# Performance work log

Measured on AMD Instinct MI355X. Metric: run time of the kernel, lower is better.

The kernel has to match this reference:

```python
import jax, jax.numpy as jnp
import numpy as np

B, S, D_IN, D_OUT, K = 4, 4096, 512, 512, 8


def setup_inputs() -> dict:
    key = jax.random.key(0)
    k1, k2, k3, k4 = jax.random.split(key, 4)
    scale_w = 1.0 / np.sqrt(D_IN)
    return {
        "x": jax.random.normal(k1, (B, S, D_IN), dtype=jnp.float32),
        "expert_weights": jax.random.normal(k2, (K, D_OUT, D_IN), dtype=jnp.float32) * scale_w,
        "expert_biases": jax.random.normal(k3, (K, D_OUT), dtype=jnp.float32) * 0.02,
        "mixer_w": jax.random.normal(k4, (K, D_IN), dtype=jnp.float32) * scale_w,
        "mixer_b": jnp.zeros((K,), dtype=jnp.float32),
    }


def reference(x, expert_weights, expert_biases, mixer_w, mixer_b):
    # Gating: coeffs = softmax(mixer(x)) over experts  -> [b, s, k]
    logits = jnp.einsum("bsi,ki->bsk", x, mixer_w) + mixer_b
    coeffs = jax.nn.softmax(logits, axis=-1)
    # Mathematically identical to fusing weights then applying them:
    #   y = einsum('bsi, bsoi -> bso', x, einsum('bsk, koi -> bsoi', coeffs, W))
    # but computed as per-expert GEMM outputs combined by coeffs, avoiding the
    # enormous [b, s, out, in] fused-weight intermediate.
    expert_out = jnp.einsum("bsi,koi->bsko", x, expert_weights)  # [b, s, k, out]
    y = jnp.einsum("bsk,bsko->bso", coeffs, expert_out)
    y = y + jnp.einsum("bsk,ko->bso", coeffs, expert_biases)
    return y
```

## Files before the change

### kernel.cpp

```cpp
#include <hip/hip_runtime.h>
#include <stdint.h>

#define NTOK 16384
#define DIN 512
#define DOUT 512
#define KE 8
#define BM 64
#define BN 128
#define BK 64

#define GATE_BLOCKS 2048
#define WCONV_BLOCKS 1024

typedef unsigned short u16;
typedef u16 u16x8 __attribute__((ext_vector_type(8)));
typedef __bf16 bf16x8 __attribute__((ext_vector_type(8)));
typedef float f32x4 __attribute__((ext_vector_type(4)));

__device__ __forceinline__ u16 f2bf(float f) {
  union { float f; unsigned u; } v; v.f = f;
  unsigned r = v.u + 0x7FFFu + ((v.u >> 16) & 1u);
  return (u16)(r >> 16);
}

#define GLOAD_LDS16(gp, lp)                                              \
  __builtin_amdgcn_global_load_lds(                                     \
      (__attribute__((address_space(1))) void*)(gp),                    \
      (__attribute__((address_space(3))) void*)(lp), 16, 0, 0)

__global__ __launch_bounds__(256) void prologue_kernel(
    const float* __restrict__ x, const float* __restrict__ mw,
    const float* __restrict__ mb, const float* __restrict__ ew,
    u16* __restrict__ xbf, u16* __restrict__ wbf, float* __restrict__ coeffs) {
  const int tid = threadIdx.x;

  if (blockIdx.x >= GATE_BLOCKS) {
    const size_t i =
        ((size_t)(blockIdx.x - GATE_BLOCKS) * 256 + tid) * 8;
    const float4 a = *(const float4*)&ew[i];
    const float4 b = *(const float4*)&ew[i + 4];
    u16x8 p;
    p[0] = f2bf(a.x); p[1] = f2bf(a.y); p[2] = f2bf(a.z); p[3] = f2bf(a.w);
    p[4] = f2bf(b.x); p[5] = f2bf(b.y); p[6] = f2bf(b.z); p[7] = f2bf(b.w);
    *(u16x8*)&wbf[i] = p;
    return;
  }

  __shared__ __align__(16) float mwS[KE * DIN];
  const int wave = tid >> 6, lane = tid & 63;

#pragma unroll
  for (int i = 0; i < 4; ++i) {
    const int idx = (tid + i * 256) * 4;
    *(float4*)&mwS[idx] = *(const float4*)&mw[idx];
  }
  float mbr[KE];
#pragma unroll
  for (int k = 0; k < KE; ++k) mbr[k] = mb[k];
  __syncthreads();

#pragma unroll
  for (int t = 0; t < 2; ++t) {
    const int tok = blockIdx.x * 8 + wave * 2 + t;
    const float* xr = x + (size_t)tok * DIN + lane * 8;
    const float4 xa = *(const float4*)xr;
    const float4 xb = *(const float4*)(xr + 4);

    u16x8 p;
    p[0] = f2bf(xa.x); p[1] = f2bf(xa.y); p[2] = f2bf(xa.z); p[3] = f2bf(xa.w);
    p[4] = f2bf(xb.x); p[5] = f2bf(xb.y); p[6] = f2bf(xb.z); p[7] = f2bf(xb.w);
    *(u16x8*)(xbf + (size_t)tok * DIN + lane * 8) = p;

    float lg[KE];
#pragma unroll
    for (int k = 0; k < KE; ++k) {
      const float* wr = &mwS[k * DIN + lane * 8];
      const float4 w0 = *(const float4*)wr;
      const float4 w1 = *(const float4*)(wr + 4);
      lg[k] = xa.x * w0.x + xa.y * w0.y + xa.z * w0.z + xa.w * w0.w +
              xb.x * w1.x + xb.y * w1.y + xb.z * w1.z + xb.w * w1.w;
    }
#pragma unroll
    for (int off = 32; off; off >>= 1)
#pragma unroll
      for (int k = 0; k < KE; ++k) lg[k] += __shfl_xor(lg[k], off);

#pragma unroll
    for (int k = 0; k < KE; ++k) lg[k] += mbr[k];
    float mx = lg[0];
#pragma unroll
    for (int k = 1; k < KE; ++k) mx = fmaxf(mx, lg[k]);
    float s = 0.f;
#pragma unroll
    for (int k = 0; k < KE; ++k) { lg[k] = __expf(lg[k] - mx); s += lg[k]; }
    const float inv = 1.f / s;
    if (lane == 0) {
      float* cp = coeffs + (size_t)tok * KE;
      float4 c0, c1;
      c0.x = lg[0] * inv; c0.y = lg[1] * inv; c0.z = lg[2] * inv; c0.w = lg[3] * inv;
      c1.x = lg[4] * inv; c1.y = lg[5] * inv; c1.z = lg[6] * inv; c1.w = lg[7] * inv;
      *(float4*)cp = c0;
      *(float4*)(cp + 4) = c1;
    }
  }
}

__global__ __launch_bounds__(256, 4) void moe_gemm_kernel(
    const u16* __restrict__ xbf, const u16* __restrict__ wbf,
    const float* __restrict__ coeffs, const float* __restrict__ ebias,
    float* __restrict__ out) {
  __shared__ __align__(16) u16 As[BM * BK];
  __shared__ __align__(16) u16 Bs[BN * BK];
  __shared__ __align__(16) float Cs[BM * KE];
  __shared__ __align__(16) float BiS[KE * BN];

  const int tid = threadIdx.x;
  const int wave = tid >> 6, lane = tid & 63;

  const int b = blockIdx.x;
  const int xcd = b & 7, s = b >> 3;
  const int m0 = (xcd * 32 + (s & 31)) * BM;
  const int n0 = (s >> 5) * BN;

  const int wm = (wave >> 1) * 32;
  const int wn = (wave & 1) * 64;

  if (tid < 128) ((float4*)Cs)[tid] = ((const float4*)(coeffs + (size_t)m0 * KE))[tid];
  {
    const int k = tid >> 5, c = (tid & 31) * 4;
    *(float4*)&BiS[k * BN + c] = *(const float4*)&ebias[k * DOUT + n0 + c];
  }

  const int lrow = lane >> 3;
  const int scol = ((lane & 7) ^ lrow) * 8;
  const u16* aBase = xbf + (size_t)(m0 + wave * 16 + lrow) * DIN + scol;

  f32x4 acc[2][4] = {};

  const int frow = lane & 15;
  const int fsel = lane >> 4;
  const int fxor = lane & 7;

  for (int e = 0; e < KE; ++e) {
    f32x4 part[2][4] = {};
    const u16* bBase = wbf + (size_t)e * DOUT * DIN +
                       (size_t)(n0 + wave * 32 + lrow) * DIN + scol;

    for (int t = 0; t < DIN / BK; ++t) {
      const int i0 = t * BK;
      __syncthreads();
#pragma unroll
      for (int j = 0; j < 2; ++j)
        GLOAD_LDS16(aBase + (size_t)(j * 8) * DIN + i0, &As[(wave * 2 + j) * 512]);
#pragma unroll
      for (int j = 0; j < 4; ++j)
        GLOAD_LDS16(bBase + (size_t)(j * 8) * DIN + i0, &Bs[(wave * 4 + j) * 512]);
      __syncthreads();
#pragma unroll
      for (int ks = 0; ks < 2; ++ks) {
        const int slot = (ks * 4 + fsel) ^ fxor;
        bf16x8 af[2], bfv[4];
#pragma unroll
        for (int mi = 0; mi < 2; ++mi)
          af[mi] = *(const bf16x8*)&As[(wm + mi * 16 + frow) * BK + slot * 8];
#pragma unroll
        for (int ni = 0; ni < 4; ++ni)
          bfv[ni] = *(const bf16x8*)&Bs[(wn + ni * 16 + frow) * BK + slot * 8];
#pragma unroll
        for (int mi = 0; mi < 2; ++mi)
#pragma unroll
          for (int ni = 0; ni < 4; ++ni)
            part[mi][ni] = __builtin_amdgcn_mfma_f32_16x16x32_bf16(
                af[mi], bfv[ni], part[mi][ni], 0, 0, 0);
      }
    }

#pragma unroll
    for (int mi = 0; mi < 2; ++mi) {
      const int rb = wm + mi * 16 + (lane >> 4) * 4;
#pragma unroll
      for (int j = 0; j < 4; ++j) {
        const float cf = Cs[(rb + j) * KE + e];
#pragma unroll
        for (int ni = 0; ni < 4; ++ni) acc[mi][ni][j] += cf * part[mi][ni][j];
      }
    }
  }

  float bcol[4][KE];
#pragma unroll
  for (int ni = 0; ni < 4; ++ni) {
    const int col = wn + ni * 16 + frow;
#pragma unroll
    for (int k = 0; k < KE; ++k) bcol[ni][k] = BiS[k * BN + col];
  }
#pragma unroll
  for (int mi = 0; mi < 2; ++mi) {
    const int rb = wm + mi * 16 + (lane >> 4) * 4;
#pragma unroll
    for (int j = 0; j < 4; ++j) {
      const int row = rb + j;
      float cr[KE];
#pragma unroll
      for (int k = 0; k < KE; ++k) cr[k] = Cs[row * KE + k];
#pragma unroll
      for (int ni = 0; ni < 4; ++ni) {
        float bias = 0.f;
#pragma unroll
        for (int k = 0; k < KE; ++k) bias += cr[k] * bcol[ni][k];
        const int col = wn + ni * 16 + frow;
        out[(size_t)(m0 + row) * DOUT + n0 + col] = acc[mi][ni][j] + bias;
      }
    }
  }
}

extern "C" void kernel_launch(void* const* d_in, const int* in_sizes, int n_in,
                              void* d_out, int out_size, void* d_ws,
                              size_t ws_size, hipStream_t stream) {
  (void)in_sizes; (void)n_in; (void)out_size; (void)ws_size;
  const float* x  = (const float*)d_in[0];
  const float* ew = (const float*)d_in[1];
  const float* eb = (const float*)d_in[2];
  const float* mw = (const float*)d_in[3];
  const float* mb = (const float*)d_in[4];
  float* out = (float*)d_out;

  u16* xbf = (u16*)d_ws;
  u16* wbf = (u16*)((char*)d_ws + (size_t)NTOK * DIN * 2);
  float* coeffs =
      (float*)((char*)d_ws + (size_t)NTOK * DIN * 2 + (size_t)KE * DOUT * DIN * 2);

  hipLaunchKernelGGL(prologue_kernel, dim3(GATE_BLOCKS + WCONV_BLOCKS),
                     dim3(256), 0, stream, x, mw, mb, ew, xbf, wbf, coeffs);
  hipLaunchKernelGGL(moe_gemm_kernel, dim3((NTOK / BM) * (DOUT / BN)), dim3(256),
                     0, stream, xbf, wbf, coeffs, eb, out);
}
```

Baseline: 189.4 us.

## Load two K-tiles per barrier pair, transpose gating coeffs, fold bias per expert

```diff
diff --git a/kernel.cpp b/kernel.cpp
--- a/kernel.cpp
+++ b/kernel.cpp
@@ -31,7 +31,7 @@
 __global__ __launch_bounds__(256) void prologue_kernel(
     const float* __restrict__ x, const float* __restrict__ mw,
     const float* __restrict__ mb, const float* __restrict__ ew,
-    u16* __restrict__ xbf, u16* __restrict__ wbf, float* __restrict__ coeffs) {
+    u16* __restrict__ xbf, u16* __restrict__ wbf, float* __restrict__ coeffsT) {
   const int tid = threadIdx.x;
 
   if (blockIdx.x >= GATE_BLOCKS) {
@@ -95,24 +95,18 @@
     for (int k = 0; k < KE; ++k) { lg[k] = __expf(lg[k] - mx); s += lg[k]; }
     const float inv = 1.f / s;
     if (lane == 0) {
-      float* cp = coeffs + (size_t)tok * KE;
-      float4 c0, c1;
-      c0.x = lg[0] * inv; c0.y = lg[1] * inv; c0.z = lg[2] * inv; c0.w = lg[3] * inv;
-      c1.x = lg[4] * inv; c1.y = lg[5] * inv; c1.z = lg[6] * inv; c1.w = lg[7] * inv;
-      *(float4*)cp = c0;
-      *(float4*)(cp + 4) = c1;
-    }
-  }
-}
-
-__global__ __launch_bounds__(256, 4) void moe_gemm_kernel(
+#pragma unroll
+      for (int k = 0; k < KE; ++k) coeffsT[(size_t)k * NTOK + tok] = lg[k] * inv;
+    }
+  }
+}
+
+__global__ __launch_bounds__(256, 3) void moe_gemm_kernel(
     const u16* __restrict__ xbf, const u16* __restrict__ wbf,
-    const float* __restrict__ coeffs, const float* __restrict__ ebias,
+    const float* __restrict__ coeffsT, const float* __restrict__ ebias,
     float* __restrict__ out) {
-  __shared__ __align__(16) u16 As[BM * BK];
-  __shared__ __align__(16) u16 Bs[BN * BK];
-  __shared__ __align__(16) float Cs[BM * KE];
-  __shared__ __align__(16) float BiS[KE * BN];
+  __shared__ __align__(16) u16 As[2][BM * BK];
+  __shared__ __align__(16) u16 Bs[2][BN * BK];
 
   const int tid = threadIdx.x;
   const int wave = tid >> 6, lane = tid & 63;
@@ -125,91 +119,89 @@
   const int wm = (wave >> 1) * 32;
   const int wn = (wave & 1) * 64;
 
-  if (tid < 128) ((float4*)Cs)[tid] = ((const float4*)(coeffs + (size_t)m0 * KE))[tid];
-  {
-    const int k = tid >> 5, c = (tid & 31) * 4;
-    *(float4*)&BiS[k * BN + c] = *(const float4*)&ebias[k * DOUT + n0 + c];
-  }
-
   const int lrow = lane >> 3;
   const int scol = ((lane & 7) ^ lrow) * 8;
   const u16* aBase = xbf + (size_t)(m0 + wave * 16 + lrow) * DIN + scol;
-
-  f32x4 acc[2][4] = {};
+  const u16* bBase0 = wbf + (size_t)(n0 + wave * 32 + lrow) * DIN + scol;
 
   const int frow = lane & 15;
   const int fsel = lane >> 4;
   const int fxor = lane & 7;
+  const int quad = lane >> 4;
+
+  f32x4 acc[2][4] = {};
 
   for (int e = 0; e < KE; ++e) {
     f32x4 part[2][4] = {};
-    const u16* bBase = wbf + (size_t)e * DOUT * DIN +
-                       (size_t)(n0 + wave * 32 + lrow) * DIN + scol;
-
-    for (int t = 0; t < DIN / BK; ++t) {
-      const int i0 = t * BK;
+    const u16* aE = aBase;
+    const u16* bE = bBase0 + (size_t)e * (DOUT * DIN);
+
+    for (int h = 0; h < 4; ++h) {
       __syncthreads();
 #pragma unroll
-      for (int j = 0; j < 2; ++j)
-        GLOAD_LDS16(aBase + (size_t)(j * 8) * DIN + i0, &As[(wave * 2 + j) * 512]);
-#pragma unroll
-      for (int j = 0; j < 4; ++j)
-        GLOAD_LDS16(bBase + (size_t)(j * 8) * DIN + i0, &Bs[(wave * 4 + j) * 512]);
+      for (int buf = 0; buf < 2; ++buf) {
+        const size_t koff = (size_t)(h * 2 + buf) * 64;
+#pragma unroll
+        for (int j = 0; j < 2; ++j)
+          GLOAD_LDS16(aE + (size_t)(j * 8) * DIN + koff,
+                      &As[buf][(wave * 2 + j) * 512]);
+#pragma unroll
+        for (int j = 0; j < 4; ++j)
+          GLOAD_LDS16(bE + (size_t)(j * 8) * DIN + koff,
+                      &Bs[buf][(wave * 4 + j) * 512]);
+      }
       __syncthreads();
-#pragma unroll
-      for (int ks = 0; ks < 2; ++ks) {
-        const int slot = (ks * 4 + fsel) ^ fxor;
-        bf16x8 af[2], bfv[4];
-#pragma unroll
-        for (int mi = 0; mi < 2; ++mi)
-          af[mi] = *(const bf16x8*)&As[(wm + mi * 16 + frow) * BK + slot * 8];
-#pragma unroll
-        for (int ni = 0; ni < 4; ++ni)
-          bfv[ni] = *(const bf16x8*)&Bs[(wn + ni * 16 + frow) * BK + slot * 8];
-#pragma unroll
-        for (int mi = 0; mi < 2; ++mi)
+
+#pragma unroll
+      for (int buf = 0; buf < 2; ++buf) {
+#pragma unroll
+        for (int ks = 0; ks < 2; ++ks) {
+          const int slot = (ks * 4 + fsel) ^ fxor;
+          bf16x8 af[2], bfv[4];
+#pragma unroll
+          for (int mi = 0; mi < 2; ++mi)
+            af[mi] = *(const bf16x8*)&As[buf][(wm + mi * 16 + frow) * BK + slot * 8];
 #pragma unroll
           for (int ni = 0; ni < 4; ++ni)
-            part[mi][ni] = __builtin_amdgcn_mfma_f32_16x16x32_bf16(
-                af[mi], bfv[ni], part[mi][ni], 0, 0, 0);
-      }
-    }
-
+            bfv[ni] = *(const bf16x8*)&Bs[buf][(wn + ni * 16 + frow) * BK + slot * 8];
+#pragma unroll
+          for (int mi = 0; mi < 2; ++mi)
+#pragma unroll
+            for (int ni = 0; ni < 4; ++ni)
+              part[mi][ni] = __builtin_amdgcn_mfma_f32_16x16x32_bf16(
+                  af[mi], bfv[ni], part[mi][ni], 0, 0, 0);
+        }
+      }
+    }
+
+    float bv[4];
+#pragma unroll
+    for (int ni = 0; ni < 4; ++ni)
+      bv[ni] = ebias[e * DOUT + n0 + wn + ni * 16 + frow];
+    const float* cT = coeffsT + (size_t)e * NTOK + m0;
 #pragma unroll
     for (int mi = 0; mi < 2; ++mi) {
-      const int rb = wm + mi * 16 + (lane >> 4) * 4;
-#pragma unroll
-      for (int j = 0; j < 4; ++j) {
-        const float cf = Cs[(rb + j) * KE + e];
-#pragma unroll
-        for (int ni = 0; ni < 4; ++ni) acc[mi][ni][j] += cf * part[mi][ni][j];
-      }
-    }
-  }
-
-  float bcol[4][KE];
-#pragma unroll
-  for (int ni = 0; ni < 4; ++ni) {
-    const int col = wn + ni * 16 + frow;
-#pragma unroll
-    for (int k = 0; k < KE; ++k) bcol[ni][k] = BiS[k * BN + col];
-  }
+      const float4 c4 = *(const float4*)&cT[wm + mi * 16 + quad * 4];
+#pragma unroll
+      for (int ni = 0; ni < 4; ++ni) {
+        acc[mi][ni][0] += c4.x * (part[mi][ni][0] + bv[ni]);
+        acc[mi][ni][1] += c4.y * (part[mi][ni][1] + bv[ni]);
+        acc[mi][ni][2] += c4.z * (part[mi][ni][2] + bv[ni]);
+        acc[mi][ni][3] += c4.w * (part[mi][ni][3] + bv[ni]);
+      }
+    }
+  }
+
 #pragma unroll
   for (int mi = 0; mi < 2; ++mi) {
-    const int rb = wm + mi * 16 + (lane >> 4) * 4;
+    const int rb = wm + mi * 16 + quad * 4;
 #pragma unroll
     for (int j = 0; j < 4; ++j) {
       const int row = rb + j;
-      float cr[KE];
-#pragma unroll
-      for (int k = 0; k < KE; ++k) cr[k] = Cs[row * KE + k];
 #pragma unroll
       for (int ni = 0; ni < 4; ++ni) {
-        float bias = 0.f;
-#pragma unroll
-        for (int k = 0; k < KE; ++k) bias += cr[k] * bcol[ni][k];
         const int col = wn + ni * 16 + frow;
-        out[(size_t)(m0 + row) * DOUT + n0 + col] = acc[mi][ni][j] + bias;
+        out[(size_t)(m0 + row) * DOUT + n0 + col] = acc[mi][ni][j];
       }
     }
   }
@@ -228,11 +220,11 @@
 
   u16* xbf = (u16*)d_ws;
   u16* wbf = (u16*)((char*)d_ws + (size_t)NTOK * DIN * 2);
-  float* coeffs =
+  float* coeffsT =
       (float*)((char*)d_ws + (size_t)NTOK * DIN * 2 + (size_t)KE * DOUT * DIN * 2);
 
   hipLaunchKernelGGL(prologue_kernel, dim3(GATE_BLOCKS + WCONV_BLOCKS),
-                     dim3(256), 0, stream, x, mw, mb, ew, xbf, wbf, coeffs);
+                     dim3(256), 0, stream, x, mw, mb, ew, xbf, wbf, coeffsT);
   hipLaunchKernelGGL(moe_gemm_kernel, dim3((NTOK / BM) * (DOUT / BN)), dim3(256),
-                     0, stream, xbf, wbf, coeffs, eb, out);
-}
+                     0, stream, xbf, wbf, coeffsT, eb, out);
+}
```

After: 181.4 us. -4.3%, faster.
